# Performance work log

Measured on AMD Instinct MI355X. Metric: run time of the kernel, lower is better.

The kernel has to match this reference:

```python
import jax, jax.numpy as jnp
import numpy as np

VOCAB, D_EMB, H, M, B, L = 50000, 512, 512, 512, 1024, 64


def _lstm_last_h(x, seqlen, kernel, bias):
    """Run BasicLSTMCell over time; return hidden state at t=seqlen (TF dynamic_rnn semantics).
    x: [B, L, D], seqlen: [B], kernel: [D+H, 4H] (i,j,f,o), bias: [4H]."""
    Bc, Lc, _ = x.shape
    xT = jnp.swapaxes(x, 0, 1)  # [L, B, D]

    def step(carry, inp):
        c, h = carry
        xt, t = inp
        gates = jnp.concatenate([xt, h], axis=-1) @ kernel + bias
        i, j, f, o = jnp.split(gates, 4, axis=-1)
        new_c = c * jax.nn.sigmoid(f + 1.0) + jax.nn.sigmoid(i) * jnp.tanh(j)
        new_h = jnp.tanh(new_c) * jax.nn.sigmoid(o)
        mask = (t < seqlen)[:, None]
        return (jnp.where(mask, new_c, c), jnp.where(mask, new_h, h)), None

    z = jnp.zeros((Bc, kernel.shape[1] // 4), x.dtype)
    (c, h), _ = jax.lax.scan(step, (z, z), (xT, jnp.arange(Lc)))
    return h


def _reverse_seq(x, seqlen):
    """tf.reverse_sequence: reverse first seqlen steps per row, keep padding in place."""
    Bc, Lc, _ = x.shape
    t = jnp.arange(Lc)[None, :]
    idx = jnp.where(t < seqlen[:, None], seqlen[:, None] - 1 - t, t)
    return jnp.take_along_axis(x, idx[:, :, None], axis=1)


def _encode(x, seqlen, k_fw, b_fw, k_bw, b_bw):
    h_fw = _lstm_last_h(x, seqlen, k_fw, b_fw)
    h_bw = _lstm_last_h(_reverse_seq(x, seqlen), seqlen, k_bw, b_bw)
    return jnp.concatenate([h_fw, h_bw], axis=1)  # [B, 2H]


def setup_inputs() -> dict:
    key = jax.random.key(0)
    ks = jax.random.split(key, 12)
    s_emb = 1.0 / np.sqrt(D_EMB)
    s_k = 1.0 / np.sqrt(D_EMB + H)
    return {
        "input1": jax.random.randint(ks[0], (B, L), 0, VOCAB, dtype=jnp.int32),
        "input2": jax.random.randint(ks[1], (B, L), 0, VOCAB, dtype=jnp.int32),
        "seqlen1": jax.random.randint(ks[2], (B,), 1, L + 1, dtype=jnp.int32),
        "seqlen2": jax.random.randint(ks[3], (B,), 1, L + 1, dtype=jnp.int32),
        "embedding": jax.random.normal(ks[4], (VOCAB, D_EMB), jnp.float32) * s_emb,
        "k_fw": jax.random.normal(ks[5], (D_EMB + H, 4 * H), jnp.float32) * s_k,
        "b_fw": jnp.zeros((4 * H,), jnp.float32),
        "k_bw": jax.random.normal(ks[6], (D_EMB + H, 4 * H), jnp.float32) * s_k,
        "b_bw": jnp.zeros((4 * H,), jnp.float32),
        "W1": jax.random.normal(ks[7], (3 * 2 * H + 1, M), jnp.float32) / np.sqrt(6 * H + 1),
        "b1": jax.random.normal(ks[8], (1, M), jnp.float32) * 0.01,
        "W2": jax.random.normal(ks[9], (M, 2), jnp.float32) / np.sqrt(M),
        "b2": jax.random.normal(ks[10], (1, 2), jnp.float32) * 0.01,
    }


def reference(input1, input2, seqlen1, seqlen2, embedding, k_fw, b_fw, k_bw, b_bw, W1, b1, W2, b2):
    x1 = embedding[input1]  # [B, L, D]
    x2 = embedding[input2]
    h1 = _encode(x1, seqlen1, k_fw, b_fw, k_bw, b_bw)  # [B, 2H]
    h2 = _encode(x2, seqlen2, k_fw, b_fw, k_bw, b_bw)
    h_dist = jnp.sum(jnp.square(h1 - h2), axis=1, keepdims=True)  # [B, 1]
    h_combined = jnp.concatenate([h1, h2, h_dist, h1 * h2], axis=1)  # [B, 6H+1]
    e1 = jax.nn.relu(h_combined @ W1 + b1)  # dropout keep_prob=1 at inference
    preds = e1 @ W2 + b2  # [B, 2]
    return preds
```

## Files before the change

kernel.cpp:

```cpp
#include <hip/hip_runtime.h>
#include <hip/hip_bf16.h>
#include <cstddef>

#define VOCAB 50000
#define D_EMB 512
#define HDIM  512
#define MDIM  512
#define BATCH 1024
#define SEQL  64
#define ROWS  2048
#define KTOT  1024
#define HC_K  3136

typedef _Float16 f16;
typedef __attribute__((ext_vector_type(8))) _Float16 f16x8;
typedef __attribute__((ext_vector_type(4))) float f32x4;

__device__ __forceinline__ float sigf(float x) {
    return 1.0f / (1.0f + __expf(-x));
}
__device__ __forceinline__ float tanh_fast(float x) {
    x = fminf(30.0f, fmaxf(-30.0f, x));
    float t = __expf(-2.0f * x);
    return (1.0f - t) / (1.0f + t);
}
__device__ __forceinline__ void glds16(const void* g, const void* lds) {
    __builtin_amdgcn_global_load_lds(
        (const __attribute__((address_space(1))) unsigned int*)g,
        (__attribute__((address_space(3))) unsigned int*)lds, 16, 0, 0);
}

__global__ __launch_bounds__(256) void conv_emb(const float* __restrict__ src,
                                                f16* __restrict__ dst, int n8) {
    int i = blockIdx.x * 256 + threadIdx.x;
    if (i >= n8) return;
    const float4* s = (const float4*)src + (size_t)i * 2;
    float4 a = s[0], b = s[1];
    f16x8 o = {(f16)a.x, (f16)a.y, (f16)a.z, (f16)a.w,
               (f16)b.x, (f16)b.y, (f16)b.z, (f16)b.w};
    *(f16x8*)&dst[(size_t)i * 8] = o;
}

__global__ __launch_bounds__(256) void pack_w(const float* __restrict__ kfw,
                                              const float* __restrict__ kbw,
                                              f16* __restrict__ Wt) {
    unsigned idx = blockIdx.x * 256 + threadIdx.x;
    int k    = idx & 1023;
    int colp = (idx >> 10) & 2047;
    int d    = idx >> 21;
    int cg = colp >> 6, g = (colp >> 4) & 3, ci = colp & 15;
    int n = cg * 16 + ci;
    const float* K = d ? kbw : kfw;
    Wt[idx] = (f16)K[(size_t)k * 2048 + g * 512 + n];
}

__global__ __launch_bounds__(256) void pack_w1(const float* __restrict__ W1,
                                               f16* __restrict__ W1t) {
    int idx = blockIdx.x * 256 + threadIdx.x;
    if (idx >= 512 * HC_K) return;
    int k = idx % HC_K, c = idx / HC_K;
    W1t[idx] = (k < 3073) ? (f16)W1[(size_t)k * MDIM + c] : (f16)0.0f;
}

__global__ __launch_bounds__(256) void sort_rows(const int* __restrict__ sl1,
                                                 const int* __restrict__ sl2,
                                                 int* __restrict__ perm,
                                                 int* __restrict__ inv,
                                                 int* __restrict__ Acnt) {
    __shared__ int s_sh[ROWS];
    int tid = threadIdx.x;
    for (int i = tid; i < ROWS; i += 256) {
        int b = i & (BATCH - 1);
        s_sh[i] = (i < BATCH) ? sl1[b] : sl2[b];
    }
    __syncthreads();
    int i = blockIdx.x * 256 + tid;
    int si = s_sh[i];
    int rank = 0;
    for (int j = 0; j < ROWS; ++j) {
        int sj = s_sh[j];
        rank += (sj > si) || (sj == si && j < i);
    }
    perm[rank] = i;
    inv[i] = rank;
    if (blockIdx.x == 0 && tid < SEQL) {
        int c = 0;
        for (int j = 0; j < ROWS; ++j) c += (s_sh[j] > tid);
        Acnt[tid] = c;
    }
}

__global__ __launch_bounds__(256, 2) void lstm_step(
    int t,
    const int* __restrict__ in1, const int* __restrict__ in2,
    const int* __restrict__ sl1, const int* __restrict__ sl2,
    const int* __restrict__ perm, const int* __restrict__ Acnt,
    const f16* __restrict__ embH,
    const f16* __restrict__ Wt,
    const float* __restrict__ bfw, const float* __restrict__ bbw,
    const f16* __restrict__ hin,
    f16* __restrict__ hout,
    float* __restrict__ cbuf)
{
    const int by  = blockIdx.y;
    if (by * 128 >= Acnt[t]) return;
    const int dir = blockIdx.z;
    const int bx  = blockIdx.x;
    const int tid = threadIdx.x;
    const int l = tid & 63, w = tid >> 6;

    __shared__ f16 Atile[2][128 * 64];
    __shared__ f16 Btile[2][128 * 64];
    __shared__ int toks[128];
    __shared__ int slens[128];

    if (tid < 128) {
        int r = perm[by * 128 + tid];
        int b = r & (BATCH - 1);
        const int* inp = (r < BATCH) ? in1 : in2;
        int s = (r < BATCH) ? sl1[b] : sl2[b];
        int tt = t;
        if (dir == 1) tt = (t < s) ? (s - 1 - t) : t;
        toks[tid]  = inp[b * SEQL + tt];
        slens[tid] = s;
    }
    __syncthreads();

    const int kg8 = (((l & 7) ^ ((l >> 3) & 7))) * 8;
    int aoffX[4]; int hoff[4]; size_t boff[4]; int dst[4];
#pragma unroll
    for (int r = 0; r < 4; ++r) {
        int row = r * 32 + w * 8 + (l >> 3);
        aoffX[r] = toks[row] * 512 + kg8;
        hoff[r]  = ((dir * ROWS + by * 128 + row) << 9) + kg8;
        boff[r]  = ((size_t)(dir * 2048 + bx * 128 + row) << 10) + kg8;
        dst[r]   = (r * 32 + w * 8) * 64;
    }

    f32x4 acc[4][4];
#pragma unroll
    for (int i = 0; i < 4; ++i)
#pragma unroll
        for (int j = 0; j < 4; ++j) acc[i][j] = (f32x4){0.f, 0.f, 0.f, 0.f};

    const int wr = w >> 1, wc = w & 1;

#pragma unroll
    for (int r = 0; r < 4; ++r) {
        glds16(embH + aoffX[r], &Atile[0][dst[r]]);
        glds16(Wt + boff[r], &Btile[0][dst[r]]);
    }
    __syncthreads();

    int cur = 0;
    for (int kt = 0; kt < 16; ++kt) {
        if (kt < 15) {
            const int kn = kt + 1;
#pragma unroll
            for (int r = 0; r < 4; ++r) {
                const f16* asrc = (kn < 8) ? (embH + aoffX[r] + kn * 64)
                                           : (hin + hoff[r] + (kn - 8) * 64);
                glds16(asrc, &Atile[cur ^ 1][dst[r]]);
                glds16(Wt + boff[r] + kn * 64, &Btile[cur ^ 1][dst[r]]);
            }
        }
#pragma unroll
        for (int kk = 0; kk < 2; ++kk) {
            f16x8 af[4], bv[4];
            const int slot = (l >> 4) + kk * 4;
#pragma unroll
            for (int fm = 0; fm < 4; ++fm) {
                int row = wr * 64 + fm * 16 + (l & 15);
                af[fm] = *(const f16x8*)&Atile[cur][row * 64 + (slot ^ (row & 7)) * 8];
            }
#pragma unroll
            for (int fn = 0; fn < 4; ++fn) {
                int col = wc * 64 + fn * 16 + (l & 15);
                bv[fn] = *(const f16x8*)&Btile[cur][col * 64 + (slot ^ (col & 7)) * 8];
            }
#pragma unroll
            for (int fm = 0; fm < 4; ++fm)
#pragma unroll
                for (int fn = 0; fn < 4; ++fn)
                    acc[fm][fn] = __builtin_amdgcn_mfma_f32_16x16x32_f16(
                        af[fm], bv[fn], acc[fm][fn], 0, 0, 0);
        }
        __syncthreads();
        cur ^= 1;
    }

    const float* bias = dir ? bbw : bfw;
    const int cell = bx * 32 + wc * 16 + (l & 15);
    float bg[4];
#pragma unroll
    for (int g = 0; g < 4; ++g) bg[g] = bias[g * 512 + cell];

#pragma unroll
    for (int fm = 0; fm < 4; ++fm) {
#pragma unroll
        for (int reg = 0; reg < 4; ++reg) {
            int rl = wr * 64 + fm * 16 + (l >> 4) * 4 + reg;
            if (t < slens[rl]) {
                size_t idx = ((size_t)(dir * ROWS + by * 128 + rl) << 9) + cell;
                float gi = acc[fm][0][reg] + bg[0];
                float gj = acc[fm][1][reg] + bg[1];
                float gf = acc[fm][2][reg] + bg[2];
                float go = acc[fm][3][reg] + bg[3];
                float cold = cbuf[idx];
                float cn = cold * sigf(gf + 1.0f) + sigf(gi) * tanh_fast(gj);
                float hn = tanh_fast(cn) * sigf(go);
                cbuf[idx] = cn;
                hout[idx] = (f16)hn;
            }
        }
    }
}

__global__ __launch_bounds__(256) void build_hc(const f16* __restrict__ hbuf0,
                                                const f16* __restrict__ hbuf1,
                                                const int* __restrict__ sl1,
                                                const int* __restrict__ sl2,
                                                const int* __restrict__ inv,
                                                f16* __restrict__ hc) {
    int b = blockIdx.x;
    int tid = threadIdx.x;
    __shared__ float red[256];
    int s1 = sl1[b], s2 = sl2[b];
    int p1 = inv[b], p2 = inv[BATCH + b];
    const f16* hf1 = (s1 & 1) ? hbuf1 : hbuf0;
    const f16* hf2 = (s2 & 1) ? hbuf1 : hbuf0;
    float d = 0.0f;
    size_t base = (size_t)b * HC_K;
    for (int k = tid; k < 1024; k += 256) {
        int dir = k >> 9, kk = k & 511;
        float h1 = (float)hf1[((size_t)(dir * ROWS + p1) << 9) + kk];
        float h2 = (float)hf2[((size_t)(dir * ROWS + p2) << 9) + kk];
        hc[base + k]        = (f16)h1;
        hc[base + 1024 + k] = (f16)h2;
        hc[base + 2049 + k] = (f16)(h1 * h2);
        float df = h1 - h2;
        d += df * df;
    }
    red[tid] = d;
    __syncthreads();
    for (int s = 128; s > 0; s >>= 1) {
        if (tid < s) red[tid] += red[tid + s];
        __syncthreads();
    }
    if (tid == 0) hc[base + 2048] = (f16)red[0];
    if (tid < HC_K - 3073) hc[base + 3073 + tid] = (f16)0.0f;
}

__global__ __launch_bounds__(256) void mlp1(const f16* __restrict__ hc,
                                            const f16* __restrict__ W1t,
                                            const float* __restrict__ b1,
                                            float* __restrict__ e1) {
    const int bx = blockIdx.x, by = blockIdx.y, tid = threadIdx.x;
    const int l = tid & 63, w = tid >> 6;
    __shared__ f16 Atile[2][64 * 64];
    __shared__ f16 Btile[2][64 * 64];

    const int kg8 = (((l & 7) ^ ((l >> 3) & 7))) * 8;
    size_t aoff[2], boff[2]; int dst[2];
#pragma unroll
    for (int g = 0; g < 2; ++g) {
        int row = g * 32 + w * 8 + (l >> 3);
        aoff[g] = (size_t)(by * 64 + row) * HC_K + kg8;
        boff[g] = (size_t)(bx * 64 + row) * HC_K + kg8;
        dst[g]  = (g * 32 + w * 8) * 64;
    }

    f32x4 acc[2][2];
#pragma unroll
    for (int i = 0; i < 2; ++i)
#pragma unroll
        for (int j = 0; j < 2; ++j) acc[i][j] = (f32x4){0.f, 0.f, 0.f, 0.f};

    const int wr = w >> 1, wc = w & 1;

#pragma unroll
    for (int g = 0; g < 2; ++g) {
        glds16(hc + aoff[g], &Atile[0][dst[g]]);
        glds16(W1t + boff[g], &Btile[0][dst[g]]);
    }
    __syncthreads();

    int cur = 0;
    for (int kt = 0; kt < HC_K / 64; ++kt) {
        if (kt < HC_K / 64 - 1) {
            const int kn = (kt + 1) * 64;
#pragma unroll
            for (int g = 0; g < 2; ++g) {
                glds16(hc + aoff[g] + kn, &Atile[cur ^ 1][dst[g]]);
                glds16(W1t + boff[g] + kn, &Btile[cur ^ 1][dst[g]]);
            }
        }
#pragma unroll
        for (int kk = 0; kk < 2; ++kk) {
            f16x8 af[2], bv[2];
            const int slot = (l >> 4) + kk * 4;
#pragma unroll
            for (int fm = 0; fm < 2; ++fm) {
                int row = wr * 32 + fm * 16 + (l & 15);
                af[fm] = *(const f16x8*)&Atile[cur][row * 64 + (slot ^ (row & 7)) * 8];
            }
#pragma unroll
            for (int fn = 0; fn < 2; ++fn) {
                int col = wc * 32 + fn * 16 + (l & 15);
                bv[fn] = *(const f16x8*)&Btile[cur][col * 64 + (slot ^ (col & 7)) * 8];
            }
#pragma unroll
            for (int fm = 0; fm < 2; ++fm)
#pragma unroll
                for (int fn = 0; fn < 2; ++fn)
                    acc[fm][fn] = __builtin_amdgcn_mfma_f32_16x16x32_f16(
                        af[fm], bv[fn], acc[fm][fn], 0, 0, 0);
        }
        __syncthreads();
        cur ^= 1;
    }

#pragma unroll
    for (int fm = 0; fm < 2; ++fm) {
#pragma unroll
        for (int fn = 0; fn < 2; ++fn) {
#pragma unroll
            for (int reg = 0; reg < 4; ++reg) {
                int r = by * 64 + wr * 32 + fm * 16 + (l >> 4) * 4 + reg;
                int c = bx * 64 + wc * 32 + fn * 16 + (l & 15);
                float v = acc[fm][fn][reg] + b1[c];
                e1[(size_t)r * MDIM + c] = v > 0.0f ? v : 0.0f;
            }
        }
    }
}

__global__ __launch_bounds__(64) void mlp2(const float* __restrict__ e1,
                                           const float* __restrict__ W2,
                                           const float* __restrict__ b2,
                                           float* __restrict__ out) {
    int b = blockIdx.x, tid = threadIdx.x;
    float p0 = 0.f, p1 = 0.f;
    for (int k = tid; k < 512; k += 64) {
        float e = e1[(size_t)b * MDIM + k];
        p0 += e * W2[2 * k];
        p1 += e * W2[2 * k + 1];
    }
    for (int off = 32; off > 0; off >>= 1) {
        p0 += __shfl_down(p0, off);
        p1 += __shfl_down(p1, off);
    }
    if (tid == 0) {
        out[2 * b]     = p0 + b2[0];
        out[2 * b + 1] = p1 + b2[1];
    }
}

extern "C" void kernel_launch(void* const* d_in, const int* in_sizes, int n_in,
                              void* d_out, int out_size, void* d_ws, size_t ws_size,
                              hipStream_t stream) {
    (void)in_sizes; (void)n_in; (void)out_size; (void)ws_size;
    const int*   in1 = (const int*)d_in[0];
    const int*   in2 = (const int*)d_in[1];
    const int*   sl1 = (const int*)d_in[2];
    const int*   sl2 = (const int*)d_in[3];
    const float* emb = (const float*)d_in[4];
    const float* kfw = (const float*)d_in[5];
    const float* bfw = (const float*)d_in[6];
    const float* kbw = (const float*)d_in[7];
    const float* bbw = (const float*)d_in[8];
    const float* W1  = (const float*)d_in[9];
    const float* b1  = (const float*)d_in[10];
    const float* W2  = (const float*)d_in[11];
    const float* b2  = (const float*)d_in[12];
    float* out = (float*)d_out;

    char* base = (char*)d_ws;
    f16*   embH = (f16*)base;
    f16*   Wt   = (f16*)(base + 51200000);
    f16*   W1t  = (f16*)(base + 59588608);
    float* cbuf = (float*)(base + 62799872);
    f16*   h0   = (f16*)(base + 71188480);
    f16*   h1   = (f16*)(base + 75382784);
    f16*   hc   = (f16*)(base + 79577088);
    float* e1   = (float*)(base + 85999616);
    int*   perm = (int*)(base + 88096768);
    int*   inv  = (int*)(base + 88104960);
    int*   Acnt = (int*)(base + 88113152);

    hipMemsetAsync(cbuf, 0, 8388608, stream);
    hipMemsetAsync(h0, 0, 4194304, stream);

    sort_rows<<<ROWS / 256, 256, 0, stream>>>(sl1, sl2, perm, inv, Acnt);
    conv_emb<<<(VOCAB * D_EMB / 8 + 255) / 256, 256, 0, stream>>>(emb, embH, VOCAB * D_EMB / 8);
    pack_w<<<(2 * 2048 * KTOT) / 256, 256, 0, stream>>>(kfw, kbw, Wt);
    pack_w1<<<(512 * HC_K + 255) / 256, 256, 0, stream>>>(W1, W1t);

    for (int t = 0; t < SEQL; ++t) {
        const f16* hi = (t & 1) ? h1 : h0;
        f16*       ho = (t & 1) ? h0 : h1;
        lstm_step<<<dim3(16, 16, 2), 256, 0, stream>>>(
            t, in1, in2, sl1, sl2, perm, Acnt, embH, Wt, bfw, bbw, hi, ho, cbuf);
    }

    build_hc<<<BATCH, 256, 0, stream>>>(h0, h1, sl1, sl2, inv, hc);
    mlp1<<<dim3(MDIM / 64, BATCH / 64), 256, 0, stream>>>(hc, W1t, b1, e1);
    mlp2<<<BATCH, 64, 0, stream>>>(e1, W2, b2, out);
}
```

Before: 1.985 ms.

## Load LSTM A operand directly into registers and vectorize sort ranking

The LSTM step GEMM no longer stages the A tile (embedding rows and previous hidden state) through shared memory. Each lane loads its MFMA A fragments straight from global memory into a register double buffer, while B still uses async global-to-LDS copies. This halves LDS traffic and footprint and may allow more blocks per CU, but A loads are now per-lane 16-byte gathers duplicated across the two column-warps, which costs more global/L2 traffic and registers. The sort kernel also packs the tie-break into a single integer key and reads shared memory as int4.

```diff
diff --git a/kernel.cpp b/kernel.cpp
--- a/kernel.cpp
+++ b/kernel.cpp
@@ -75,17 +75,25 @@
     }
     __syncthreads();
     int i = blockIdx.x * 256 + tid;
-    int si = s_sh[i];
+    int key = (s_sh[i] << 12) - i;
     int rank = 0;
-    for (int j = 0; j < ROWS; ++j) {
-        int sj = s_sh[j];
-        rank += (sj > si) || (sj == si && j < i);
+#pragma unroll 4
+    for (int j = 0; j < ROWS; j += 4) {
+        int4 v = *(const int4*)&s_sh[j];
+        rank += ((v.x << 12) - (j + 0)) > key;
+        rank += ((v.y << 12) - (j + 1)) > key;
+        rank += ((v.z << 12) - (j + 2)) > key;
+        rank += ((v.w << 12) - (j + 3)) > key;
     }
     perm[rank] = i;
     inv[i] = rank;
     if (blockIdx.x == 0 && tid < SEQL) {
         int c = 0;
-        for (int j = 0; j < ROWS; ++j) c += (s_sh[j] > tid);
+#pragma unroll 4
+        for (int j = 0; j < ROWS; j += 4) {
+            int4 v = *(const int4*)&s_sh[j];
+            c += (v.x > tid) + (v.y > tid) + (v.z > tid) + (v.w > tid);
+        }
         Acnt[tid] = c;
     }
 }
@@ -109,7 +117,6 @@
     const int tid = threadIdx.x;
     const int l = tid & 63, w = tid >> 6;
 
-    __shared__ f16 Atile[2][128 * 64];
     __shared__ f16 Btile[2][128 * 64];
     __shared__ int toks[128];
     __shared__ int slens[128];
@@ -127,14 +134,23 @@
     __syncthreads();
 
     const int kg8 = (((l & 7) ^ ((l >> 3) & 7))) * 8;
-    int aoffX[4]; int hoff[4]; size_t boff[4]; int dst[4];
+    size_t boff[4]; int dstB[4];
 #pragma unroll
     for (int r = 0; r < 4; ++r) {
         int row = r * 32 + w * 8 + (l >> 3);
-        aoffX[r] = toks[row] * 512 + kg8;
-        hoff[r]  = ((dir * ROWS + by * 128 + row) << 9) + kg8;
-        boff[r]  = ((size_t)(dir * 2048 + bx * 128 + row) << 10) + kg8;
-        dst[r]   = (r * 32 + w * 8) * 64;
+        boff[r] = ((size_t)(dir * 2048 + bx * 128 + row) << 10) + kg8;
+        dstB[r] = (r * 32 + w * 8) * 64;
+    }
+
+    const int wr = w >> 1, wc = w & 1;
+
+    const int koff = (l >> 4) * 8;
+    const f16* aEmb[4]; const f16* aH[4];
+#pragma unroll
+    for (int fm = 0; fm < 4; ++fm) {
+        int row = wr * 64 + fm * 16 + (l & 15);
+        aEmb[fm] = embH + (size_t)toks[row] * 512 + koff;
+        aH[fm]   = hin + ((size_t)(dir * ROWS + by * 128 + row) << 9) + koff;
     }
 
     f32x4 acc[4][4];
@@ -143,36 +159,37 @@
 #pragma unroll
         for (int j = 0; j < 4; ++j) acc[i][j] = (f32x4){0.f, 0.f, 0.f, 0.f};
 
-    const int wr = w >> 1, wc = w & 1;
-
-#pragma unroll
-    for (int r = 0; r < 4; ++r) {
-        glds16(embH + aoffX[r], &Atile[0][dst[r]]);
-        glds16(Wt + boff[r], &Btile[0][dst[r]]);
-    }
+    f16x8 aF[2][4][2];
+
+#pragma unroll
+    for (int fm = 0; fm < 4; ++fm)
+#pragma unroll
+        for (int kk = 0; kk < 2; ++kk)
+            aF[0][fm][kk] = *(const f16x8*)(aEmb[fm] + kk * 32);
+#pragma unroll
+    for (int r = 0; r < 4; ++r)
+        glds16(Wt + boff[r], &Btile[0][dstB[r]]);
     __syncthreads();
 
-    int cur = 0;
+#pragma unroll
     for (int kt = 0; kt < 16; ++kt) {
+        const int cur = kt & 1;
         if (kt < 15) {
-            const int kn = kt + 1;
-#pragma unroll
-            for (int r = 0; r < 4; ++r) {
-                const f16* asrc = (kn < 8) ? (embH + aoffX[r] + kn * 64)
-                                           : (hin + hoff[r] + (kn - 8) * 64);
-                glds16(asrc, &Atile[cur ^ 1][dst[r]]);
-                glds16(Wt + boff[r] + kn * 64, &Btile[cur ^ 1][dst[r]]);
-            }
+#pragma unroll
+            for (int r = 0; r < 4; ++r)
+                glds16(Wt + boff[r] + (kt + 1) * 64, &Btile[cur ^ 1][dstB[r]]);
+#pragma unroll
+            for (int fm = 0; fm < 4; ++fm)
+#pragma unroll
+                for (int kk = 0; kk < 2; ++kk)
+                    aF[cur ^ 1][fm][kk] = (kt + 1 < 8)
+                        ? *(const f16x8*)(aEmb[fm] + (kt + 1) * 64 + kk * 32)
+                        : *(const f16x8*)(aH[fm] + (kt + 1 - 8) * 64 + kk * 32);
         }
 #pragma unroll
         for (int kk = 0; kk < 2; ++kk) {
-            f16x8 af[4], bv[4];
+            f16x8 bv[4];
             const int slot = (l >> 4) + kk * 4;
-#pragma unroll
-            for (int fm = 0; fm < 4; ++fm) {
-                int row = wr * 64 + fm * 16 + (l & 15);
-                af[fm] = *(const f16x8*)&Atile[cur][row * 64 + (slot ^ (row & 7)) * 8];
-            }
 #pragma unroll
             for (int fn = 0; fn < 4; ++fn) {
                 int col = wc * 64 + fn * 16 + (l & 15);
@@ -183,10 +200,9 @@
 #pragma unroll
                 for (int fn = 0; fn < 4; ++fn)
                     acc[fm][fn] = __builtin_amdgcn_mfma_f32_16x16x32_f16(
-                        af[fm], bv[fn], acc[fm][fn], 0, 0, 0);
+                        aF[cur][fm][kk], bv[fn], acc[fm][fn], 0, 0, 0);
         }
         __syncthreads();
-        cur ^= 1;
     }
 
     const float* bias = dir ? bbw : bfw;
```

After: 3.063 ms. +54.3%, slower.
